# Kernel tuning notes

Hardware: AMD Instinct MI355X
Metric: run time of the kernel (lower is better)

## Reference

```python
import math
import jax, jax.numpy as jnp
import numpy as np

RCR = 5.2   # radial cutoff
RCA = 3.5   # angular cutoff
B, N, T, KR, KA = 256, 24, 4, 16, 32

# static index tables (depend only on N)
_NIDX = np.array([[j for j in range(N) if j != i] for i in range(N)])  # [N, N-1] neighbors excluding self
_I1, _I2 = np.triu_indices(N - 1, k=1)                                  # pair combinations, P = C(N-1,2)


def setup_inputs() -> dict:
    key = jax.random.key(0)
    k1, k2 = jax.random.split(key)
    coords = jax.random.normal(k1, (B, N, 3), dtype=jnp.float32)
    atom_types = jax.random.randint(k2, (N,), 0, T)
    EtaR = jnp.full((T, KR), 16.0, dtype=jnp.float32)
    ShfR = jnp.tile(jnp.linspace(0.9, 4.95, KR, dtype=jnp.float32), (T, 1))
    Zeta = jnp.full((T, KA), 32.0, dtype=jnp.float32)
    ShfZ = jnp.tile(jnp.tile(jnp.linspace(0.9, 3.525, 8, dtype=jnp.float32), 4), (T, 1))
    EtaA = jnp.full((T, KA), 8.0, dtype=jnp.float32)
    ShfA = jnp.tile(jnp.repeat(jnp.linspace(0.3927, 2.7489, 4, dtype=jnp.float32), 8), (T, 1))
    return dict(coords=coords, atom_types=atom_types, EtaR=EtaR, ShfR=ShfR,
                Zeta=Zeta, ShfZ=ShfZ, EtaA=EtaA, ShfA=ShfA)


def reference(coords, atom_types, EtaR, ShfR, Zeta, ShfZ, EtaA, ShfA):
    # pairwise vectors excluding self: rij[b,i,k] = coords[b,i] - coords[b, j_k], j_k != i
    rij = coords[:, :, None, :] - coords[:, _NIDX, :]                      # [B,N,N-1,3]

    # gather per-atom parameter rows: [N, K] -> broadcast as [1,N,1,K]
    etaR = EtaR[atom_types][None, :, None, :]
    shfR = ShfR[atom_types][None, :, None, :]
    zeta = Zeta[atom_types][None, :, None, :]
    shfZ = ShfZ[atom_types][None, :, None, :]
    etaA = EtaA[atom_types][None, :, None, :]
    shfA = ShfA[atom_types][None, :, None, :]

    # ---- radial G2 ----
    dij = jnp.linalg.norm(rij, axis=3)                                     # [B,N,N-1]
    fij = 0.5 * (jnp.cos(dij * (math.pi / RCR)) + 1.0)
    g2 = jnp.sum(jnp.exp(-etaR * (dij[..., None] - shfR) ** 2) * fij[..., None], axis=2)  # [B,N,KR]

    # ---- angular G3 (ANI) ----
    r12 = rij[:, :, _I1]                                                   # [B,N,P,3]
    r13 = rij[:, :, _I2]
    d12 = jnp.linalg.norm(r12, axis=3)                                     # [B,N,P]
    d13 = jnp.linalg.norm(r13, axis=3)
    f12 = 0.5 * (jnp.cos(d12 * (math.pi / RCA)) + 1.0)
    f13 = 0.5 * (jnp.cos(d13 * (math.pi / RCA)) + 1.0)
    cosine = jnp.einsum('bnpc,bnpc->bnp', r12, r13) / (d12 * d13)
    cosine = jnp.clip(cosine, -1.0 + 1e-7, 1.0 - 1e-7)  # numerical guard for acos
    cosang = jnp.cos(jnp.arccos(cosine)[..., None] - shfA)                 # [B,N,P,KA]
    g3 = jnp.sum(
        2.0 ** (1.0 - zeta) * (1.0 + cosang) ** zeta
        * jnp.exp(-etaA * (0.5 * (d12 + d13)[..., None] - shfZ) ** 2)
        * (f12 * f13)[..., None],
        axis=2)                                                            # [B,N,KA]

    return jnp.concatenate((g2, g3), axis=2)                               # [B,N,KR+KA]
```

## Files before the change

### kernel.cpp

```cpp
#include <hip/hip_runtime.h>


constexpr int CB = 256;
constexpr int CN = 24;
constexpr int CKR = 16;
constexpr int CKA = 32;
constexpr int NN = 23;
constexpr int NP = 253;
constexpr int KOUT = CKR + CKA;
#define LOG2E 1.44269504088896340736f

struct PairTab { unsigned char pa[256]; unsigned char pb[256]; };
static constexpr PairTab make_pairs() {
    PairTab t{};
    int p = 0;
    for (int i = 0; i < NN; ++i)
        for (int j = i + 1; j < NN; ++j) {
            t.pa[p] = (unsigned char)i; t.pb[p] = (unsigned char)j; ++p;
        }
    for (; p < 256; ++p) { t.pa[p] = 0; t.pb[p] = 0; }
    return t;
}
__constant__ PairTab cPairs = make_pairs();

template<int MASK, int BIT, int HALF>
__device__ inline void red_level(float* acc, int lane) {
    const bool hi = (lane >> BIT) & 1;
#pragma unroll
    for (int j = 0; j < HALF; ++j) {
        float send = hi ? acc[j] : acc[j + HALF];
        float recv = __shfl_xor(send, MASK, 64);
        float keep = hi ? acc[j + HALF] : acc[j];
        acc[j] = keep + recv;
    }
}

__global__ __launch_bounds__(256) void ani_kernel(
    const float* __restrict__ coords, const int* __restrict__ atom_types,
    const float* __restrict__ EtaR, const float* __restrict__ ShfR,
    const float* __restrict__ Zeta, const float* __restrict__ ShfZ,
    const float* __restrict__ EtaA, const float* __restrict__ ShfA,
    float* __restrict__ out)
{
    __shared__ float s_rx[4][NN], s_ry[4][NN], s_rz[4][NN];
    __shared__ float s_d [4][NN], s_inv[4][NN], s_fA[4][NN], s_fR[4][NN];

    const int wv   = threadIdx.x >> 6;
    const int lane = threadIdx.x & 63;
    const int row  = blockIdx.x * 4 + wv;
    const int b    = row / CN;
    const int i    = row - b * CN;

    const float cix = coords[row*3+0], ciy = coords[row*3+1], ciz = coords[row*3+2];
    if (lane < NN) {
        const int j   = lane + (lane >= i ? 1 : 0);
        const int idx = (b * CN + j) * 3;
        const float dx = cix - coords[idx+0];
        const float dy = ciy - coords[idx+1];
        const float dz = ciz - coords[idx+2];
        const float d  = __builtin_amdgcn_sqrtf(dx*dx + dy*dy + dz*dz);
        s_rx[wv][lane] = dx; s_ry[wv][lane] = dy; s_rz[wv][lane] = dz;
        s_d  [wv][lane] = d;
        s_inv[wv][lane] = __builtin_amdgcn_rcpf(d);
        s_fR[wv][lane] = 0.5f * (__cosf(d * (float)(3.14159265358979323846/5.2)) + 1.0f);
        s_fA[wv][lane] = 0.5f * (__cosf(d * (float)(3.14159265358979323846/3.5)) + 1.0f);
    }
    __builtin_amdgcn_wave_barrier();

    const int t = atom_types[i];

    {
        const int k = lane & 15, g = lane >> 4;
        const float eta = EtaR[t*CKR + k] * LOG2E;
        const float shf = ShfR[t*CKR + k];
        float acc = 0.0f;
        for (int j = g; j < NN; j += 4) {
            const float x = s_d[wv][j] - shf;
            acc += __builtin_amdgcn_exp2f(-eta * x * x) * s_fR[wv][j];
        }
        acc += __shfl_xor(acc, 16, 64);
        acc += __shfl_xor(acc, 32, 64);
        if (lane < CKR) out[row * KOUT + k] = acc;
    }

    float4 pd[4];
    #pragma unroll
    for (int it = 0; it < 4; ++it) {
        const int p = lane + it * 64;
        const int a = cPairs.pa[p], c = cPairs.pb[p];
        const float d12 = s_d[wv][a], d13 = s_d[wv][c];
        const float dot = s_rx[wv][a]*s_rx[wv][c]
                        + s_ry[wv][a]*s_ry[wv][c]
                        + s_rz[wv][a]*s_rz[wv][c];
        float cosv = dot * (s_inv[wv][a] * s_inv[wv][c]);
        cosv = fminf(fmaxf(cosv, -1.0f + 1e-7f), 1.0f - 1e-7f);
        const float sinv = __builtin_amdgcn_sqrtf(1.0f - cosv * cosv);
        const float avg  = 0.5f * (d12 + d13);
        const float ff2  = (p < NP) ? 2.0f * s_fA[wv][a] * s_fA[wv][c] : 0.0f;
        pd[it] = make_float4(cosv, sinv, avg, ff2);
    }

    const float* __restrict__ Zt = ShfZ + t*CKA;
    const float* __restrict__ At = ShfA + t*CKA;
    const int kk = lane & 31;
    const bool okl = (Zeta[t*CKA + kk] == 32.0f)
                  && (EtaA[t*CKA + kk] == EtaA[t*CKA])
                  && (Zt[kk] == Zt[kk & 7])
                  && (At[kk] == At[kk & 24]);
    const bool fast = __all(okl);

    if (fast) {
        const float cgau = -EtaA[t*CKA] * LOG2E;
        float Zv[8], cAv[4], sAv[4];
        #pragma unroll
        for (int z = 0; z < 8; ++z) Zv[z] = Zt[z];
        #pragma unroll
        for (int a = 0; a < 4; ++a) {
            const float sh = At[a * 8];
            cAv[a] = __cosf(sh); sAv[a] = __sinf(sh);
        }
        float acc[32];
        #pragma unroll
        for (int k = 0; k < 32; ++k) acc[k] = 0.0f;

        #pragma unroll
        for (int it = 0; it < 4; ++it) {
            const float4 q = pd[it];
            float G[8];
            #pragma unroll
            for (int z = 0; z < 8; ++z) {
                const float x = q.z - Zv[z];
                G[z] = __builtin_amdgcn_exp2f(cgau * x * x);
            }
            #pragma unroll
            for (int a = 0; a < 4; ++a) {
                const float cosang = q.x * cAv[a] + q.y * sAv[a];
                const float hh  = 0.5f * cosang + 0.5f;
                const float h2 = hh*hh, h4 = h2*h2, h8 = h4*h4, h16 = h8*h8;
                const float Pa = (h16 * h16) * q.w;
                #pragma unroll
                for (int z = 0; z < 8; ++z)
                    acc[a*8 + z] = fmaf(Pa, G[z], acc[a*8 + z]);
            }
        }

        red_level<1, 0, 16>(acc, lane);
        red_level<2, 1,  8>(acc, lane);
        red_level<4, 2,  4>(acc, lane);
        red_level<8, 3,  2>(acc, lane);
        red_level<16, 4, 1>(acc, lane);
        acc[0] += __shfl_xor(acc[0], 32, 64);
        if (lane < 32) {
            const int k = ((lane & 1) << 4) | ((lane & 2) << 2) | (lane & 4)
                        | ((lane & 8) >> 2) | ((lane & 16) >> 4);
            out[row * KOUT + CKR + k] = acc[0];
        }
    } else {
        const int k = lane & 31, h = lane >> 5;
        const float zeta  = Zeta[t*CKA + k];
        const float shfZ  = Zt[k];
        const float etaAl = EtaA[t*CKA + k] * LOG2E;
        const float shfA  = At[k];
        const float cA = __cosf(shfA), sA = __sinf(shfA);
        float acc = 0.0f;
        for (int p = h; p < NP; p += 2) {
            const int a = cPairs.pa[p], c = cPairs.pb[p];
            const float d12 = s_d[wv][a], d13 = s_d[wv][c];
            const float dot = s_rx[wv][a]*s_rx[wv][c]
                            + s_ry[wv][a]*s_ry[wv][c]
                            + s_rz[wv][a]*s_rz[wv][c];
            float cosv = dot * (s_inv[wv][a] * s_inv[wv][c]);
            cosv = fminf(fmaxf(cosv, -1.0f + 1e-7f), 1.0f - 1e-7f);
            const float sinv = __builtin_amdgcn_sqrtf(1.0f - cosv * cosv);
            const float cosang = cosv * cA + sinv * sA;
            const float hh  = 0.5f * cosang + 0.5f;
            const float l2h = __log2f(hh);
            const float x   = 0.5f * (d12 + d13) - shfZ;
            const float e   = zeta * l2h - etaAl * x * x;
            acc += (2.0f * s_fA[wv][a] * s_fA[wv][c]) * __builtin_amdgcn_exp2f(e);
        }
        acc += __shfl_xor(acc, 32, 64);
        if (lane < CKA) out[row * KOUT + CKR + k] = acc;
    }
}

extern "C" void kernel_launch(void* const* d_in, const int* in_sizes, int n_in,
                              void* d_out, int out_size, void* d_ws, size_t ws_size,
                              hipStream_t stream) {
    const float* coords     = (const float*)d_in[0];
    const int*   atom_types = (const int*)  d_in[1];
    const float* EtaR       = (const float*)d_in[2];
    const float* ShfR       = (const float*)d_in[3];
    const float* Zeta       = (const float*)d_in[4];
    const float* ShfZ       = (const float*)d_in[5];
    const float* EtaA       = (const float*)d_in[6];
    const float* ShfA       = (const float*)d_in[7];
    float* out = (float*)d_out;

    dim3 grid((CB * CN) / 4), block(256);
    hipLaunchKernelGGL(ani_kernel, grid, block, 0, stream,
                       coords, atom_types, EtaR, ShfR, Zeta, ShfZ, EtaA, ShfA, out);
}
```

Measured before the change: 78.58 us.

## Share per-molecule distance matrix across atoms and use law of cosines

Measured after the change: 78.49 us. About the same (-0.1%).

```diff
diff --git a/kernel.cpp b/kernel.cpp
--- a/kernel.cpp
+++ b/kernel.cpp
@@ -8,6 +8,7 @@
 constexpr int NN = 23;
 constexpr int NP = 253;
 constexpr int KOUT = CKR + CKA;
+constexpr int LDM = 25;
 #define LOG2E 1.44269504088896340736f
 
 struct PairTab { unsigned char pa[256]; unsigned char pb[256]; };
@@ -42,145 +43,158 @@
     const float* __restrict__ EtaA, const float* __restrict__ ShfA,
     float* __restrict__ out)
 {
-    __shared__ float s_rx[4][NN], s_ry[4][NN], s_rz[4][NN];
-    __shared__ float s_d [4][NN], s_inv[4][NN], s_fA[4][NN], s_fR[4][NN];
-
-    const int wv   = threadIdx.x >> 6;
-    const int lane = threadIdx.x & 63;
-    const int row  = blockIdx.x * 4 + wv;
-    const int b    = row / CN;
-    const int i    = row - b * CN;
-
-    const float cix = coords[row*3+0], ciy = coords[row*3+1], ciz = coords[row*3+2];
-    if (lane < NN) {
-        const int j   = lane + (lane >= i ? 1 : 0);
-        const int idx = (b * CN + j) * 3;
-        const float dx = cix - coords[idx+0];
-        const float dy = ciy - coords[idx+1];
-        const float dz = ciz - coords[idx+2];
+    __shared__ float sc[CN][3];
+    __shared__ float sD [CN*LDM];
+    __shared__ float sI [CN*LDM];
+    __shared__ float sFA[CN*LDM];
+    __shared__ float sFR[CN*LDM];
+
+    const int tid  = threadIdx.x;
+    const int wv   = tid >> 6;
+    const int lane = tid & 63;
+    const int m    = blockIdx.x >> 1;
+    const int h    = blockIdx.x & 1;
+
+    if (tid < CN * 3) sc[tid / 3][tid % 3] = coords[m * CN * 3 + tid];
+    __syncthreads();
+
+    for (int p = tid; p < CN * CN; p += 256) {
+        const int j = p / CN, k = p - j * CN;
+        const float dx = sc[j][0] - sc[k][0];
+        const float dy = sc[j][1] - sc[k][1];
+        const float dz = sc[j][2] - sc[k][2];
         const float d  = __builtin_amdgcn_sqrtf(dx*dx + dy*dy + dz*dz);
-        s_rx[wv][lane] = dx; s_ry[wv][lane] = dy; s_rz[wv][lane] = dz;
-        s_d  [wv][lane] = d;
-        s_inv[wv][lane] = __builtin_amdgcn_rcpf(d);
-        s_fR[wv][lane] = 0.5f * (__cosf(d * (float)(3.14159265358979323846/5.2)) + 1.0f);
-        s_fA[wv][lane] = 0.5f * (__cosf(d * (float)(3.14159265358979323846/3.5)) + 1.0f);
+        const int o = j * LDM + k;
+        sD [o] = d;
+        sI [o] = __builtin_amdgcn_rcpf(d);
+        sFA[o] = 0.5f * (__cosf(d * (float)(3.14159265358979323846/3.5)) + 1.0f);
+        sFR[o] = 0.5f * (__cosf(d * (float)(3.14159265358979323846/5.2)) + 1.0f);
     }
-    __builtin_amdgcn_wave_barrier();
-
-    const int t = atom_types[i];
-
-    {
-        const int k = lane & 15, g = lane >> 4;
-        const float eta = EtaR[t*CKR + k] * LOG2E;
-        const float shf = ShfR[t*CKR + k];
-        float acc = 0.0f;
-        for (int j = g; j < NN; j += 4) {
-            const float x = s_d[wv][j] - shf;
-            acc += __builtin_amdgcn_exp2f(-eta * x * x) * s_fR[wv][j];
-        }
-        acc += __shfl_xor(acc, 16, 64);
-        acc += __shfl_xor(acc, 32, 64);
-        if (lane < CKR) out[row * KOUT + k] = acc;
-    }
-
-    float4 pd[4];
-    #pragma unroll
-    for (int it = 0; it < 4; ++it) {
-        const int p = lane + it * 64;
-        const int a = cPairs.pa[p], c = cPairs.pb[p];
-        const float d12 = s_d[wv][a], d13 = s_d[wv][c];
-        const float dot = s_rx[wv][a]*s_rx[wv][c]
-                        + s_ry[wv][a]*s_ry[wv][c]
-                        + s_rz[wv][a]*s_rz[wv][c];
-        float cosv = dot * (s_inv[wv][a] * s_inv[wv][c]);
-        cosv = fminf(fmaxf(cosv, -1.0f + 1e-7f), 1.0f - 1e-7f);
-        const float sinv = __builtin_amdgcn_sqrtf(1.0f - cosv * cosv);
-        const float avg  = 0.5f * (d12 + d13);
-        const float ff2  = (p < NP) ? 2.0f * s_fA[wv][a] * s_fA[wv][c] : 0.0f;
-        pd[it] = make_float4(cosv, sinv, avg, ff2);
-    }
-
-    const float* __restrict__ Zt = ShfZ + t*CKA;
-    const float* __restrict__ At = ShfA + t*CKA;
-    const int kk = lane & 31;
-    const bool okl = (Zeta[t*CKA + kk] == 32.0f)
-                  && (EtaA[t*CKA + kk] == EtaA[t*CKA])
-                  && (Zt[kk] == Zt[kk & 7])
-                  && (At[kk] == At[kk & 24]);
-    const bool fast = __all(okl);
-
-    if (fast) {
-        const float cgau = -EtaA[t*CKA] * LOG2E;
-        float Zv[8], cAv[4], sAv[4];
-        #pragma unroll
-        for (int z = 0; z < 8; ++z) Zv[z] = Zt[z];
-        #pragma unroll
-        for (int a = 0; a < 4; ++a) {
-            const float sh = At[a * 8];
-            cAv[a] = __cosf(sh); sAv[a] = __sinf(sh);
-        }
-        float acc[32];
-        #pragma unroll
-        for (int k = 0; k < 32; ++k) acc[k] = 0.0f;
-
+    __syncthreads();
+
+    #pragma unroll 1
+    for (int r = 0; r < 3; ++r) {
+        const int i   = h * 12 + wv * 3 + r;
+        const int row = m * CN + i;
+        const int t   = atom_types[i];
+        const int i25 = i * LDM;
+
+        {
+            const int k = lane & 15, g = lane >> 4;
+            const float eta = EtaR[t*CKR + k] * LOG2E;
+            const float shf = ShfR[t*CKR + k];
+            float acc = 0.0f;
+            for (int n = g; n < NN; n += 4) {
+                const int j = n + (n >= i ? 1 : 0);
+                const float x = sD[i25 + j] - shf;
+                acc += __builtin_amdgcn_exp2f(-eta * x * x) * sFR[i25 + j];
+            }
+            acc += __shfl_xor(acc, 16, 64);
+            acc += __shfl_xor(acc, 32, 64);
+            if (lane < CKR) out[row * KOUT + k] = acc;
+        }
+
+        float4 pd[4];
         #pragma unroll
         for (int it = 0; it < 4; ++it) {
-            const float4 q = pd[it];
-            float G[8];
-            #pragma unroll
-            for (int z = 0; z < 8; ++z) {
-                const float x = q.z - Zv[z];
-                G[z] = __builtin_amdgcn_exp2f(cgau * x * x);
-            }
-            #pragma unroll
-            for (int a = 0; a < 4; ++a) {
-                const float cosang = q.x * cAv[a] + q.y * sAv[a];
-                const float hh  = 0.5f * cosang + 0.5f;
-                const float h2 = hh*hh, h4 = h2*h2, h8 = h4*h4, h16 = h8*h8;
-                const float Pa = (h16 * h16) * q.w;
-                #pragma unroll
-                for (int z = 0; z < 8; ++z)
-                    acc[a*8 + z] = fmaf(Pa, G[z], acc[a*8 + z]);
-            }
-        }
-
-        red_level<1, 0, 16>(acc, lane);
-        red_level<2, 1,  8>(acc, lane);
-        red_level<4, 2,  4>(acc, lane);
-        red_level<8, 3,  2>(acc, lane);
-        red_level<16, 4, 1>(acc, lane);
-        acc[0] += __shfl_xor(acc[0], 32, 64);
-        if (lane < 32) {
-            const int k = ((lane & 1) << 4) | ((lane & 2) << 2) | (lane & 4)
-                        | ((lane & 8) >> 2) | ((lane & 16) >> 4);
-            out[row * KOUT + CKR + k] = acc[0];
-        }
-    } else {
-        const int k = lane & 31, h = lane >> 5;
-        const float zeta  = Zeta[t*CKA + k];
-        const float shfZ  = Zt[k];
-        const float etaAl = EtaA[t*CKA + k] * LOG2E;
-        const float shfA  = At[k];
-        const float cA = __cosf(shfA), sA = __sinf(shfA);
-        float acc = 0.0f;
-        for (int p = h; p < NP; p += 2) {
-            const int a = cPairs.pa[p], c = cPairs.pb[p];
-            const float d12 = s_d[wv][a], d13 = s_d[wv][c];
-            const float dot = s_rx[wv][a]*s_rx[wv][c]
-                            + s_ry[wv][a]*s_ry[wv][c]
-                            + s_rz[wv][a]*s_rz[wv][c];
-            float cosv = dot * (s_inv[wv][a] * s_inv[wv][c]);
+            const int p  = lane + it * 64;
+            const int n1 = cPairs.pa[p], n2 = cPairs.pb[p];
+            const int j  = n1 + (n1 >= i ? 1 : 0);
+            const int k2 = n2 + (n2 >= i ? 1 : 0);
+            const float d12 = sD[i25 + j],  d13 = sD[i25 + k2];
+            const float djk = sD[j * LDM + k2];
+            const float i12 = sI[i25 + j],  i13 = sI[i25 + k2];
+            float cosv = (d12*d12 + d13*d13 - djk*djk) * (0.5f * i12 * i13);
             cosv = fminf(fmaxf(cosv, -1.0f + 1e-7f), 1.0f - 1e-7f);
             const float sinv = __builtin_amdgcn_sqrtf(1.0f - cosv * cosv);
-            const float cosang = cosv * cA + sinv * sA;
-            const float hh  = 0.5f * cosang + 0.5f;
-            const float l2h = __log2f(hh);
-            const float x   = 0.5f * (d12 + d13) - shfZ;
-            const float e   = zeta * l2h - etaAl * x * x;
-            acc += (2.0f * s_fA[wv][a] * s_fA[wv][c]) * __builtin_amdgcn_exp2f(e);
-        }
-        acc += __shfl_xor(acc, 32, 64);
-        if (lane < CKA) out[row * KOUT + CKR + k] = acc;
+            const float avg  = 0.5f * (d12 + d13);
+            const float ff2  = (p < NP) ? 2.0f * sFA[i25 + j] * sFA[i25 + k2] : 0.0f;
+            pd[it] = make_float4(cosv, sinv, avg, ff2);
+        }
+
+        const float* __restrict__ Zt = ShfZ + t*CKA;
+        const float* __restrict__ At = ShfA + t*CKA;
+        const int kk = lane & 31;
+        const bool okl = (Zeta[t*CKA + kk] == 32.0f)
+                      && (EtaA[t*CKA + kk] == EtaA[t*CKA])
+                      && (Zt[kk] == Zt[kk & 7])
+                      && (At[kk] == At[kk & 24]);
+        const bool fast = __all(okl);
+
+        if (fast) {
+            const float cgau = -EtaA[t*CKA] * LOG2E;
+            float Zv[8], cAv[4], sAv[4];
+            #pragma unroll
+            for (int z = 0; z < 8; ++z) Zv[z] = Zt[z];
+            #pragma unroll
+            for (int a = 0; a < 4; ++a) {
+                const float sh = At[a * 8];
+                cAv[a] = __cosf(sh); sAv[a] = __sinf(sh);
+            }
+            float acc[32];
+            #pragma unroll
+            for (int k = 0; k < 32; ++k) acc[k] = 0.0f;
+
+            #pragma unroll
+            for (int it = 0; it < 4; ++it) {
+                const float4 q = pd[it];
+                float G[8];
+                #pragma unroll
+                for (int z = 0; z < 8; ++z) {
+                    const float x = q.z - Zv[z];
+                    G[z] = __builtin_amdgcn_exp2f(cgau * x * x);
+                }
+                #pragma unroll
+                for (int a = 0; a < 4; ++a) {
+                    const float cosang = q.x * cAv[a] + q.y * sAv[a];
+                    const float hh  = 0.5f * cosang + 0.5f;
+                    const float h2 = hh*hh, h4 = h2*h2, h8 = h4*h4, h16 = h8*h8;
+                    const float Pa = (h16 * h16) * q.w;
+                    #pragma unroll
+                    for (int z = 0; z < 8; ++z)
+                        acc[a*8 + z] = fmaf(Pa, G[z], acc[a*8 + z]);
+                }
+            }
+
+            red_level<1, 0, 16>(acc, lane);
+            red_level<2, 1,  8>(acc, lane);
+            red_level<4, 2,  4>(acc, lane);
+            red_level<8, 3,  2>(acc, lane);
+            red_level<16, 4, 1>(acc, lane);
+            acc[0] += __shfl_xor(acc[0], 32, 64);
+            if (lane < 32) {
+                const int k = ((lane & 1) << 4) | ((lane & 2) << 2) | (lane & 4)
+                            | ((lane & 8) >> 2) | ((lane & 16) >> 4);
+                out[row * KOUT + CKR + k] = acc[0];
+            }
+        } else {
+            const int k = lane & 31, hh2 = lane >> 5;
+            const float zeta  = Zeta[t*CKA + k];
+            const float shfZ  = Zt[k];
+            const float etaAl = EtaA[t*CKA + k] * LOG2E;
+            const float shfA  = At[k];
+            const float cA = __cosf(shfA), sA = __sinf(shfA);
+            float acc = 0.0f;
+            for (int p = hh2; p < NP; p += 2) {
+                const int n1 = cPairs.pa[p], n2 = cPairs.pb[p];
+                const int j  = n1 + (n1 >= i ? 1 : 0);
+                const int k2 = n2 + (n2 >= i ? 1 : 0);
+                const float d12 = sD[i25 + j],  d13 = sD[i25 + k2];
+                const float djk = sD[j * LDM + k2];
+                const float i12 = sI[i25 + j],  i13 = sI[i25 + k2];
+                float cosv = (d12*d12 + d13*d13 - djk*djk) * (0.5f * i12 * i13);
+                cosv = fminf(fmaxf(cosv, -1.0f + 1e-7f), 1.0f - 1e-7f);
+                const float sinv = __builtin_amdgcn_sqrtf(1.0f - cosv * cosv);
+                const float cosang = cosv * cA + sinv * sA;
+                const float hhp = 0.5f * cosang + 0.5f;
+                const float l2h = __log2f(hhp);
+                const float x   = 0.5f * (d12 + d13) - shfZ;
+                const float e   = zeta * l2h - etaAl * x * x;
+                acc += (2.0f * sFA[i25 + j] * sFA[i25 + k2]) * __builtin_amdgcn_exp2f(e);
+            }
+            acc += __shfl_xor(acc, 32, 64);
+            if (lane < CKA) out[row * KOUT + CKR + k] = acc;
+        }
     }
 }
 
@@ -197,7 +211,7 @@
     const float* ShfA       = (const float*)d_in[7];
     float* out = (float*)d_out;
 
-    dim3 grid((CB * CN) / 4), block(256);
+    dim3 grid(CB * 2), block(256);
     hipLaunchKernelGGL(ani_kernel, grid, block, 0, stream,
                        coords, atom_types, EtaR, ShfR, Zeta, ShfZ, EtaA, ShfA, out);
 }
```
